# Kernel optimization log

Measured on AMD Instinct MI355X. Metric: run time of the kernel, lower is better.

Reference implementation:

```python
import jax, jax.numpy as jnp
import numpy as np

B = 4096      # graphs
N = 21        # nodes per graph (EEG electrodes)
CIN = 512
H1 = 1024
H2 = 1024
COUT = 512
R = 4         # SE reduction
RANK = 10     # nodevec rank
EPS = 1e-5
THRESH = 0.1


def setup_inputs() -> dict:
    key = jax.random.key(0)
    ks = jax.random.split(key, 16)
    p = lambda i, shape, s=0.02: (jax.random.normal(ks[i], shape, jnp.float32) * s)
    return {
        "x": jax.random.normal(ks[0], (B * N, CIN), jnp.float32),
        "batch": jnp.arange(B * N, dtype=jnp.int32) // N,
        "nodevec1": jax.random.normal(ks[1], (N, RANK), jnp.float32),
        "nodevec2": jax.random.normal(ks[2], (RANK, N), jnp.float32),
        "se_w1": p(3, (CIN, CIN // R), 0.05),
        "se_w2": p(4, (CIN // R, CIN), 0.05),
        "W1": p(5, (CIN, H1)), "b1": jnp.zeros((H1,), jnp.float32),
        "W2": p(6, (H1, H2)), "b2": jnp.zeros((H2,), jnp.float32),
        "W3": p(7, (H2, COUT)), "b3": jnp.zeros((COUT,), jnp.float32),
        "bn1_g": jnp.ones((H1,), jnp.float32), "bn1_b": jnp.zeros((H1,), jnp.float32),
        "bn2_g": jnp.ones((H2,), jnp.float32), "bn2_b": jnp.zeros((H2,), jnp.float32),
        "bn3_g": jnp.ones((COUT,), jnp.float32), "bn3_b": jnp.zeros((COUT,), jnp.float32),
        "rs1_w": p(8, (CIN, H1)), "rs1_b": jnp.zeros((H1,), jnp.float32),
        "fc_w": p(9, (COUT, 2 * COUT)), "fc_b": jnp.zeros((2 * COUT,), jnp.float32),
    }


def _batchnorm(h, g, b):
    # training-mode BN: biased batch stats over the node dimension
    m = h.mean(0)
    v = h.var(0)
    return (h - m) * jax.lax.rsqrt(v + EPS) * g + b


def _gcn(A, h, W, b):
    # GCNConv with precomputed normalized+thresholded weights:
    # out = A_block_diag @ (h @ W) + b, done densely per graph since A is 21x21
    hm = (h @ W).reshape(B, N, -1)                 # [B, N, Cout]
    agg = jnp.einsum('ij,bjc->bic', A, hm)         # message passing per graph
    return agg.reshape(B * N, -1) + b


def _forward(x, batch, nodevec1, nodevec2, se_w1, se_w2,
             W1, b1, W2, b2, W3, b3,
             bn1_g, bn1_b, bn2_g, bn2_b, bn3_g, bn3_b,
             rs1_w, rs1_b, fc_w, fc_b):
    # SE layer on [B, N, C]: channel-wise gating from node-mean features
    x3 = x.reshape(B, N, CIN)
    y = jax.nn.sigmoid(jax.nn.relu(x3.mean(1) @ se_w1) @ se_w2)   # [B, C]
    xg = (x3 * y[:, None, :]).reshape(B * N, CIN)
    # adaptive adjacency: sigmoid(nv1 @ nv2), symmetric normalize, threshold
    adp = jax.nn.sigmoid(nodevec1 @ nodevec2)                      # [N, N]
    at = adp + jnp.eye(N, dtype=adp.dtype)
    deg = at.sum(1)
    dinv = jnp.where(deg > 0, deg ** -0.5, 0.0)
    A = dinv[:, None] * at * dinv[None, :]
    A = jnp.where(A > THRESH, A, 0.0)
    # layer 1 (+ projected residual, BN, relu; dropout omitted = eval)
    h = _batchnorm(_gcn(A, xg, W1, b1), bn1_g, bn1_b) + (xg @ rs1_w + rs1_b)
    h = jax.nn.relu(h)
    # layer 2 (h1 == h2 -> identity residual)
    h = jax.nn.relu(_batchnorm(_gcn(A, h, W2, b2), bn2_g, bn2_b) + h)
    # layer 3
    h = _batchnorm(_gcn(A, h, W3, b3), bn3_g, bn3_b)
    # global mean pool by graph id
    ssum = jax.ops.segment_sum(h, batch, num_segments=B)
    cnt = jax.ops.segment_sum(jnp.ones((h.shape[0], 1), h.dtype), batch, num_segments=B)
    pooled = ssum / cnt
    return pooled @ fc_w + fc_b                                    # [B, 2*COUT]


def reference(x, batch, nodevec1, nodevec2, se_w1, se_w2,
              W1, b1, W2, b2, W3, b3,
              bn1_g, bn1_b, bn2_g, bn2_b, bn3_g, bn3_b,
              rs1_w, rs1_b, fc_w, fc_b):
    return _forward(x, batch, nodevec1, nodevec2, se_w1, se_w2,
                    W1, b1, W2, b2, W3, b3,
                    bn1_g, bn1_b, bn2_g, bn2_b, bn3_g, bn3_b,
                    rs1_w, rs1_b, fc_w, fc_b)
```

## Files before the change

kernel.cpp:

```cpp
#include <hip/hip_runtime.h>

typedef _Float16 f16;
typedef f16 f16x2 __attribute__((ext_vector_type(2)));
typedef f16 f16x8 __attribute__((ext_vector_type(8)));
typedef float f32x4 __attribute__((ext_vector_type(4)));
typedef const void __attribute__((address_space(1)))* gas1;
typedef void __attribute__((address_space(3)))* las3;

#define NB 4096
#define NN 21
#define MROWS (NB*NN)
#define CIN 512
#define H1C 1024
#define H2C 1024
#define COUTC 512

__global__ void k_adj(const float* __restrict__ nv1, const float* __restrict__ nv2,
                      float* __restrict__ Aout) {
  __shared__ float at[21][21];
  __shared__ float dinv[21];
  int t = threadIdx.x;
  if (t < 441) {
    int i = t / 21, j = t % 21;
    float s = 0.f;
    #pragma unroll
    for (int r = 0; r < 10; r++) s += nv1[i*10 + r] * nv2[r*21 + j];
    float v = 1.f / (1.f + expf(-s));
    if (i == j) v += 1.f;
    at[i][j] = v;
  }
  __syncthreads();
  if (t < 21) {
    float d = 0.f;
    #pragma unroll
    for (int j = 0; j < 21; j++) d += at[t][j];
    dinv[t] = d > 0.f ? rsqrtf(d) : 0.f;
  }
  __syncthreads();
  if (t < 441) {
    int i = t / 21, j = t % 21;
    float a = dinv[i] * at[i][j] * dinv[j];
    Aout[t] = a > 0.1f ? a : 0.f;
  }
}

__global__ void k_transpose(const float* __restrict__ src, f16* __restrict__ dst,
                            int K, int N) {
  __shared__ float tile[32][33];
  int n0 = blockIdx.x * 32, k0 = blockIdx.y * 32;
  int tx = threadIdx.x, ty = threadIdx.y;
  #pragma unroll
  for (int i = 0; i < 4; i++)
    tile[ty + 8*i][tx] = src[(size_t)(k0 + ty + 8*i) * N + n0 + tx];
  __syncthreads();
  #pragma unroll
  for (int i = 0; i < 4; i++)
    dst[(size_t)(n0 + ty + 8*i) * K + k0 + tx] = (f16)tile[tx][ty + 8*i];
}

__global__ void k_mean(const float* __restrict__ x, float* __restrict__ xm) {
  int b = blockIdx.x, t = threadIdx.x;
  for (int c = t; c < CIN; c += 256) {
    float s = 0.f;
    #pragma unroll
    for (int n = 0; n < NN; n++) s += x[((size_t)b*NN + n)*CIN + c];
    xm[(size_t)b*CIN + c] = s * (1.f/21.f);
  }
}

__global__ void k_se1(const float* __restrict__ xm, const float* __restrict__ w1,
                      float* __restrict__ y1) {
  __shared__ float row[CIN];
  int b = blockIdx.x, t = threadIdx.x;
  for (int k = t; k < CIN; k += 128) row[k] = xm[(size_t)b*CIN + k];
  __syncthreads();
  float acc = 0.f;
  for (int k = 0; k < CIN; k++) acc += row[k] * w1[(size_t)k*128 + t];
  y1[(size_t)b*128 + t] = fmaxf(acc, 0.f);
}

__global__ void k_se2(const float* __restrict__ y1, const float* __restrict__ w2,
                      float* __restrict__ y) {
  __shared__ float row[128];
  int b = blockIdx.x, t = threadIdx.x;
  if (t < 128) row[t] = y1[(size_t)b*128 + t];
  __syncthreads();
  float acc = 0.f;
  for (int k = 0; k < 128; k++) acc += row[k] * w2[(size_t)k*CIN + t];
  y[(size_t)b*CIN + t] = 1.f / (1.f + expf(-acc));
}

__global__ void k_gate(const float* __restrict__ x, const float* __restrict__ y,
                       f16* __restrict__ xg) {
  size_t i8 = (size_t)blockIdx.x * 256 + threadIdx.x;
  size_t base = i8 * 8;
  int r = (int)(base >> 9);
  int c = (int)(base & 511);
  int b = r / 21;
  const float4* xp = (const float4*)(x + base);
  const float4* yp = (const float4*)(y + (size_t)b*CIN + c);
  float4 a0 = xp[0], a1 = xp[1];
  float4 g0 = yp[0], g1 = yp[1];
  f16x8 o;
  o[0] = (f16)(a0.x * g0.x); o[1] = (f16)(a0.y * g0.y);
  o[2] = (f16)(a0.z * g0.z); o[3] = (f16)(a0.w * g0.w);
  o[4] = (f16)(a1.x * g1.x); o[5] = (f16)(a1.y * g1.y);
  o[6] = (f16)(a1.z * g1.z); o[7] = (f16)(a1.w * g1.w);
  *(f16x8*)(xg + base) = o;
}

#define GBM 128
#define GBN 256
#define BUFB 49152

template<int MODE>
__global__ __launch_bounds__(512, 1)
void k_gemm8(const f16* __restrict__ A, const f16* __restrict__ BT,
             f16* __restrict__ C1, f16* __restrict__ C2,
             const float* __restrict__ bias, float* __restrict__ Cf,
             int N, int K, int lgn) {
  __shared__ __align__(16) char lds[3 * BUFB];
  const int tid = threadIdx.x;
  const int nwg = gridDim.x;
  const int g = blockIdx.x;
  const int swz = (g & 7) * (nwg >> 3) + (g >> 3);
  const int bn = swz & ((1 << lgn) - 1);
  const int bm = swz >> lgn;
  const int lane = tid & 63;
  const int wid = tid >> 6;
  const int wr = wid >> 2;
  const int wc = wid & 3;
  const int fr = lane & 15;
  const int kg = lane >> 4;

  size_t srcOff[6]; int ldsOff[6];
  #pragma unroll
  for (int j = 0; j < 6; j++) {
    int gid = j * 512 + tid;
    if (gid < 1024) {
      int row = gid >> 3, gr = gid & 7;
      int gsw = gr ^ (row & 7);
      srcOff[j] = (size_t)(bm * GBM + row) * K + gsw * 8;
      ldsOff[j] = gid * 16;
    } else {
      int bgid = gid - 1024;
      int row = bgid >> 3, gr = bgid & 7;
      int gsw = gr ^ (row & 7);
      srcOff[j] = (size_t)(bn * GBN + row) * K + gsw * 8;
      ldsOff[j] = 16384 + bgid * 16;
    }
  }

  int aOff[4], axor[4], bOff[4], bxor[4];
  #pragma unroll
  for (int m = 0; m < 4; m++) {
    int row = wr*64 + m*16 + fr;
    aOff[m] = row * 128; axor[m] = row & 7;
  }
  #pragma unroll
  for (int n = 0; n < 4; n++) {
    int row = wc*64 + n*16 + fr;
    bOff[n] = 16384 + row * 128; bxor[n] = row & 7;
  }

  f32x4 acc[4][4];
  #pragma unroll
  for (int m = 0; m < 4; m++)
    #pragma unroll
    for (int n = 0; n < 4; n++)
      #pragma unroll
      for (int r = 0; r < 4; r++) acc[m][n][r] = 0.f;

  auto STAGE3 = [&](int t2, int sbuf, int j0) {
    char* dst = (char*)lds + sbuf * BUFB;
    const size_t kof = (size_t)t2 * 64;
    #pragma unroll
    for (int j = 0; j < 3; j++) {
      int jj = j0 + j;
      const f16* src = (jj < 2 ? A : BT) + srcOff[jj] + kof;
      __builtin_amdgcn_global_load_lds((gas1)src, (las3)(dst + ldsOff[jj]), 16, 0, 0);
    }
  };

  const int NT = K >> 6;
  STAGE3(0, 0, 0); STAGE3(0, 0, 3);
  STAGE3(1, 1, 0); STAGE3(1, 1, 3);
  asm volatile("s_waitcnt vmcnt(6)" ::: "memory");
  asm volatile("s_barrier" ::: "memory");

  for (int t = 0; t < NT; t++) {
    const int cb = t % 3;
    const int sb = (t + 2) % 3;
    const char* rb = (const char*)lds + cb * BUFB;
    const bool ds = (t + 2) < NT;

    f16x8 av[4], bv[4];
    #pragma unroll
    for (int m = 0; m < 4; m++)
      av[m] = *(const f16x8*)(rb + aOff[m] + ((kg ^ axor[m]) << 4));
    #pragma unroll
    for (int n = 0; n < 4; n++)
      bv[n] = *(const f16x8*)(rb + bOff[n] + ((kg ^ bxor[n]) << 4));
    if (ds) STAGE3(t + 2, sb, 0);
    asm volatile("s_barrier" ::: "memory");
    __builtin_amdgcn_s_setprio(1);
    #pragma unroll
    for (int m = 0; m < 4; m++)
      #pragma unroll
      for (int n = 0; n < 4; n++)
        acc[m][n] = __builtin_amdgcn_mfma_f32_16x16x32_f16(av[m], bv[n], acc[m][n], 0, 0, 0);
    __builtin_amdgcn_s_setprio(0);
    asm volatile("s_barrier" ::: "memory");

    #pragma unroll
    for (int m = 0; m < 4; m++)
      av[m] = *(const f16x8*)(rb + aOff[m] + (((4 + kg) ^ axor[m]) << 4));
    #pragma unroll
    for (int n = 0; n < 4; n++)
      bv[n] = *(const f16x8*)(rb + bOff[n] + (((4 + kg) ^ bxor[n]) << 4));
    if (ds) STAGE3(t + 2, sb, 3);
    asm volatile("s_barrier" ::: "memory");
    __builtin_amdgcn_s_setprio(1);
    #pragma unroll
    for (int m = 0; m < 4; m++)
      #pragma unroll
      for (int n = 0; n < 4; n++)
        acc[m][n] = __builtin_amdgcn_mfma_f32_16x16x32_f16(av[m], bv[n], acc[m][n], 0, 0, 0);
    __builtin_amdgcn_s_setprio(0);
    if (ds) asm volatile("s_waitcnt vmcnt(6)" ::: "memory");
    else    asm volatile("s_waitcnt vmcnt(0)" ::: "memory");
    asm volatile("s_barrier" ::: "memory");
  }

  const int crow = bm * GBM + wr * 64 + ((lane >> 4) << 2);
  const int ccol = bn * GBN + wc * 64 + fr;
  if constexpr (MODE == 0) {
    #pragma unroll
    for (int m = 0; m < 4; m++)
      #pragma unroll
      for (int n = 0; n < 4; n++)
        #pragma unroll
        for (int r = 0; r < 4; r++)
          C1[(size_t)(crow + m*16 + r) * N + (ccol + n*16)] = (f16)acc[m][n][r];
  } else if constexpr (MODE == 1) {
    f16* Cp = (bn < 4) ? C1 : C2;
    const int cc = (bn & 3) * 256 + wc * 64 + fr;
    #pragma unroll
    for (int m = 0; m < 4; m++)
      #pragma unroll
      for (int n = 0; n < 4; n++)
        #pragma unroll
        for (int r = 0; r < 4; r++)
          Cp[(size_t)(crow + m*16 + r) * 1024 + (cc + n*16)] = (f16)acc[m][n][r];
  } else {
    #pragma unroll
    for (int n = 0; n < 4; n++) {
      float bb = bias[ccol + n*16];
      #pragma unroll
      for (int m = 0; m < 4; m++)
        #pragma unroll
        for (int r = 0; r < 4; r++)
          Cf[(size_t)(crow + m*16 + r) * N + (ccol + n*16)] = acc[m][n][r] + bb;
    }
  }
}

__global__ __launch_bounds__(256)
void k_mix(f16* __restrict__ t, const float* __restrict__ Aadj,
           float* __restrict__ psum, float* __restrict__ psq, int C) {
  __shared__ float A[441];
  int b = blockIdx.x, tid = threadIdx.x;
  for (int i = tid; i < 441; i += 256) A[i] = Aadj[i];
  __syncthreads();
  int c0 = (blockIdx.y * 256 + tid) * 2;
  size_t base = (size_t)b * NN * C + c0;
  float vx[21], vy[21];
  #pragma unroll
  for (int j = 0; j < 21; j++) {
    f16x2 v = *(const f16x2*)(t + base + (size_t)j * C);
    vx[j] = (float)v[0]; vy[j] = (float)v[1];
  }
  float s0 = 0.f, s1 = 0.f, q0 = 0.f, q1 = 0.f;
  #pragma unroll
  for (int i = 0; i < 21; i++) {
    float a0 = 0.f, a1 = 0.f;
    #pragma unroll
    for (int j = 0; j < 21; j++) {
      float w = A[i*21 + j];
      a0 = fmaf(w, vx[j], a0);
      a1 = fmaf(w, vy[j], a1);
    }
    f16x2 o; o[0] = (f16)a0; o[1] = (f16)a1;
    *(f16x2*)(t + base + (size_t)i * C) = o;
    s0 += a0; s1 += a1;
    q0 = fmaf(a0, a0, q0); q1 = fmaf(a1, a1, q1);
  }
  float2 sv; sv.x = s0; sv.y = s1;
  float2 qv; qv.x = q0; qv.y = q1;
  *(float2*)(psum + (size_t)b * C + c0) = sv;
  *(float2*)(psq  + (size_t)b * C + c0) = qv;
}

__global__ void k_reduce(const float* __restrict__ ps, const float* __restrict__ pq,
                         float* __restrict__ rs, float* __restrict__ rq, int C) {
  int c = blockIdx.x * 256 + threadIdx.x;
  int py = blockIdx.y;
  float s = 0.f, q = 0.f;
  for (int p = py*128; p < py*128 + 128; p++) {
    s += ps[(size_t)p*C + c];
    q += pq[(size_t)p*C + c];
  }
  rs[(size_t)py*C + c] = s;
  rq[(size_t)py*C + c] = q;
}

__global__ void k_bnparams(const float* __restrict__ psum, const float* __restrict__ psq,
                           const float* __restrict__ gamma, const float* __restrict__ beta,
                           const float* __restrict__ resbias,
                           float* __restrict__ scale, float* __restrict__ shift,
                           int C, int npart) {
  int c = blockIdx.x * 256 + threadIdx.x;
  float s = 0.f, q = 0.f;
  for (int p = 0; p < npart; p++) { s += psum[(size_t)p*C + c]; q += psq[(size_t)p*C + c]; }
  const float Minv = 1.f / (float)MROWS;
  float mean = s * Minv;
  float var = q * Minv - mean * mean;
  float sc = gamma[c] * rsqrtf(var + 1e-5f);
  float sh = beta[c] - mean * sc;
  if (resbias) sh += resbias[c];
  scale[c] = sc; shift[c] = sh;
}

__global__ void k_finalize(const f16* __restrict__ g, const f16* __restrict__ res,
                           f16* __restrict__ dst, const float* __restrict__ scale,
                           const float* __restrict__ shift, int cmask) {
  size_t i8 = (size_t)blockIdx.x * 256 + threadIdx.x;
  size_t base = i8 * 8;
  int c = (int)(base & (size_t)cmask);
  f16x8 gv = *(const f16x8*)(g + base);
  f16x8 rv = *(const f16x8*)(res + base);
  f16x8 o;
  #pragma unroll
  for (int j = 0; j < 8; j++) {
    float v = (float)gv[j] * scale[c + j] + shift[c + j] + (float)rv[j];
    o[j] = (f16)fmaxf(v, 0.f);
  }
  *(f16x8*)(dst + base) = o;
}

__global__ void k_pool(const f16* __restrict__ g3, const float* __restrict__ scale,
                       const float* __restrict__ shift, f16* __restrict__ pooled) {
  int b = blockIdx.x, t = threadIdx.x;
  for (int c = t; c < COUTC; c += 256) {
    float s = 0.f;
    #pragma unroll
    for (int n = 0; n < NN; n++) s += (float)g3[((size_t)b*NN + n)*COUTC + c];
    pooled[(size_t)b*COUTC + c] = (f16)((s * (1.f/21.f)) * scale[c] + shift[c]);
  }
}

extern "C" void kernel_launch(void* const* d_in, const int* in_sizes, int n_in,
                              void* d_out, int out_size, void* d_ws, size_t ws_size,
                              hipStream_t stream) {
  const float* x     = (const float*)d_in[0];
  const float* nv1   = (const float*)d_in[2];
  const float* nv2   = (const float*)d_in[3];
  const float* se_w1 = (const float*)d_in[4];
  const float* se_w2 = (const float*)d_in[5];
  const float* W1    = (const float*)d_in[6];
  const float* W2    = (const float*)d_in[8];
  const float* W3    = (const float*)d_in[10];
  const float* bn1g  = (const float*)d_in[12];
  const float* bn1b  = (const float*)d_in[13];
  const float* bn2g  = (const float*)d_in[14];
  const float* bn2b  = (const float*)d_in[15];
  const float* bn3g  = (const float*)d_in[16];
  const float* bn3b  = (const float*)d_in[17];
  const float* rs1w  = (const float*)d_in[18];
  const float* rs1b  = (const float*)d_in[19];
  const float* fcw   = (const float*)d_in[20];
  const float* fcb   = (const float*)d_in[21];
  float* out = (float*)d_out;

  char* ws = (char*)d_ws;
  size_t off = 0;
  auto alloc = [&](size_t bytes) -> char* {
    char* p = ws + off;
    off = (off + bytes + 255) & ~(size_t)255;
    return p;
  };

  float* A_adj = (float*)alloc(441 * 4);
  f16* W1R  = (f16*)alloc((size_t)2048 * CIN * 2);
  f16* W2T  = (f16*)alloc((size_t)H2C * H1C * 2);
  f16* W3T  = (f16*)alloc((size_t)COUTC * H2C * 2);
  f16* FCWT = (f16*)alloc((size_t)1024 * COUTC * 2);
  float* xm = (float*)alloc((size_t)NB * CIN * 4);
  float* y1 = (float*)alloc((size_t)NB * 128 * 4);
  float* yv = (float*)alloc((size_t)NB * CIN * 4);
  float* psum = (float*)alloc((size_t)NB * 1024 * 4);
  float* psq  = (float*)alloc((size_t)NB * 1024 * 4);
  float* rsum = (float*)alloc((size_t)32 * 1024 * 4);
  float* rsq  = (float*)alloc((size_t)32 * 1024 * 4);
  float* sc1 = (float*)alloc(1024 * 4);
  float* sh1 = (float*)alloc(1024 * 4);
  float* sc2 = (float*)alloc(1024 * 4);
  float* sh2 = (float*)alloc(1024 * 4);
  float* sc3 = (float*)alloc(1024 * 4);
  float* sh3 = (float*)alloc(1024 * 4);
  f16* pooled = (f16*)alloc((size_t)NB * COUTC * 2);
  f16* P1 = (f16*)alloc((size_t)MROWS * 512 * 2);
  f16* P2 = (f16*)alloc((size_t)MROWS * 1024 * 2);
  f16* P3 = (f16*)alloc((size_t)MROWS * 1024 * 2);
  (void)ws_size; (void)in_sizes; (void)n_in; (void)out_size;

  k_adj<<<1, 512, 0, stream>>>(nv1, nv2, A_adj);
  k_transpose<<<dim3(32, 16), dim3(32, 8), 0, stream>>>(W1,   W1R,                    512, 1024);
  k_transpose<<<dim3(32, 16), dim3(32, 8), 0, stream>>>(rs1w, W1R + (size_t)1024*512, 512, 1024);
  k_transpose<<<dim3(32, 32), dim3(32, 8), 0, stream>>>(W2,   W2T,  1024, 1024);
  k_transpose<<<dim3(16, 32), dim3(32, 8), 0, stream>>>(W3,   W3T,  1024, 512);
  k_transpose<<<dim3(32, 16), dim3(32, 8), 0, stream>>>(fcw,  FCWT, 512, 1024);

  k_mean<<<NB, 256, 0, stream>>>(x, xm);
  k_se1<<<NB, 128, 0, stream>>>(xm, se_w1, y1);
  k_se2<<<NB, 512, 0, stream>>>(y1, se_w2, yv);
  k_gate<<<21504, 256, 0, stream>>>(x, yv, P1);

  k_gemm8<1><<<672*8, 512, 0, stream>>>(P1, W1R, P2, P3, nullptr, nullptr, 2048, 512, 3);
  k_mix<<<dim3(NB, 2), 256, 0, stream>>>(P2, A_adj, psum, psq, 1024);
  k_reduce<<<dim3(4, 32), 256, 0, stream>>>(psum, psq, rsum, rsq, 1024);
  k_bnparams<<<4, 256, 0, stream>>>(rsum, rsq, bn1g, bn1b, rs1b, sc1, sh1, 1024, 32);
  k_finalize<<<43008, 256, 0, stream>>>(P2, P3, P3, sc1, sh1, 1023);

  k_gemm8<0><<<672*4, 512, 0, stream>>>(P3, W2T, P2, nullptr, nullptr, nullptr, 1024, 1024, 2);
  k_mix<<<dim3(NB, 2), 256, 0, stream>>>(P2, A_adj, psum, psq, 1024);
  k_reduce<<<dim3(4, 32), 256, 0, stream>>>(psum, psq, rsum, rsq, 1024);
  k_bnparams<<<4, 256, 0, stream>>>(rsum, rsq, bn2g, bn2b, nullptr, sc2, sh2, 1024, 32);
  k_finalize<<<43008, 256, 0, stream>>>(P2, P3, P2, sc2, sh2, 1023);

  k_gemm8<0><<<672*2, 512, 0, stream>>>(P2, W3T, P1, nullptr, nullptr, nullptr, 512, 1024, 1);
  k_mix<<<dim3(NB, 1), 256, 0, stream>>>(P1, A_adj, psum, psq, 512);
  k_reduce<<<dim3(2, 32), 256, 0, stream>>>(psum, psq, rsum, rsq, 512);
  k_bnparams<<<2, 256, 0, stream>>>(rsum, rsq, bn3g, bn3b, nullptr, sc3, sh3, 512, 32);

  k_pool<<<NB, 256, 0, stream>>>(P1, sc3, sh3, pooled);
  k_gemm8<2><<<32*4, 512, 0, stream>>>(pooled, FCWT, nullptr, nullptr, fcb, out, 1024, 512, 2);
}
```

Measured before the change: 1.215 ms.

## Reassociate adjacency mix before GEMMs, fuse BN stats into GEMM epilogue, pipeline LDS reads

Uses A(hW) = (Ah)W to apply the 21x21 adjacency mix before the GEMM on the narrower input: in place on the 512-wide gated input for layer 1, and fused with BN-finalize/relu in a new k_finmix for layer 3. The GEMM epilogue now computes per-tile column sums and sums of squares for the batch-norm statistics, so the separate mix+stats passes for layers 1 and 3 go away. The gemm main loop is restructured to double-buffer LDS fragment reads across half-steps with fewer barriers. Layer 1 now runs as two separate GEMMs instead of one concatenated GEMM. Fp16 rounding happens at different points, which may shift numerics slightly.

```diff
diff --git a/kernel.cpp b/kernel.cpp
--- a/kernel.cpp
+++ b/kernel.cpp
@@ -11,9 +11,6 @@
 #define NN 21
 #define MROWS (NB*NN)
 #define CIN 512
-#define H1C 1024
-#define H2C 1024
-#define COUTC 512
 
 __global__ void k_adj(const float* __restrict__ nv1, const float* __restrict__ nv2,
                       float* __restrict__ Aout) {
@@ -116,9 +113,9 @@
 template<int MODE>
 __global__ __launch_bounds__(512, 1)
 void k_gemm8(const f16* __restrict__ A, const f16* __restrict__ BT,
-             f16* __restrict__ C1, f16* __restrict__ C2,
-             const float* __restrict__ bias, float* __restrict__ Cf,
-             int N, int K, int lgn) {
+             f16* __restrict__ C1, const float* __restrict__ bias,
+             float* __restrict__ Cf, float* __restrict__ psum,
+             float* __restrict__ psq, int N, int K, int lgn) {
   __shared__ __align__(16) char lds[3 * BUFB];
   const int tid = threadIdx.x;
   const int nwg = gridDim.x;
@@ -181,60 +178,70 @@
       __builtin_amdgcn_global_load_lds((gas1)src, (las3)(dst + ldsOff[jj]), 16, 0, 0);
     }
   };
-
+  auto READF = [&](f16x8* avv, f16x8* bvv, const char* rb, int s) {
+    #pragma unroll
+    for (int m = 0; m < 4; m++)
+      avv[m] = *(const f16x8*)(rb + aOff[m] + (((s*4 + kg) ^ axor[m]) << 4));
+    #pragma unroll
+    for (int n = 0; n < 4; n++)
+      bvv[n] = *(const f16x8*)(rb + bOff[n] + (((s*4 + kg) ^ bxor[n]) << 4));
+  };
+
+  f16x8 av0[4], bv0[4], av1[4], bv1[4];
   const int NT = K >> 6;
   STAGE3(0, 0, 0); STAGE3(0, 0, 3);
   STAGE3(1, 1, 0); STAGE3(1, 1, 3);
   asm volatile("s_waitcnt vmcnt(6)" ::: "memory");
   asm volatile("s_barrier" ::: "memory");
+  READF(av0, bv0, (const char*)lds, 0);
 
   for (int t = 0; t < NT; t++) {
-    const int cb = t % 3;
+    const char* rb  = (const char*)lds + (t % 3) * BUFB;
+    const char* rbn = (const char*)lds + ((t + 1) % 3) * BUFB;
     const int sb = (t + 2) % 3;
-    const char* rb = (const char*)lds + cb * BUFB;
-    const bool ds = (t + 2) < NT;
-
-    f16x8 av[4], bv[4];
+    const bool stg  = (t + 2) < NT;
+    const bool more = (t + 1) < NT;
+
+    if (stg) STAGE3(t + 2, sb, 0);
+    READF(av1, bv1, rb, 1);
+    __builtin_amdgcn_s_setprio(1);
     #pragma unroll
     for (int m = 0; m < 4; m++)
-      av[m] = *(const f16x8*)(rb + aOff[m] + ((kg ^ axor[m]) << 4));
-    #pragma unroll
-    for (int n = 0; n < 4; n++)
-      bv[n] = *(const f16x8*)(rb + bOff[n] + ((kg ^ bxor[n]) << 4));
-    if (ds) STAGE3(t + 2, sb, 0);
-    asm volatile("s_barrier" ::: "memory");
+      #pragma unroll
+      for (int n = 0; n < 4; n++)
+        acc[m][n] = __builtin_amdgcn_mfma_f32_16x16x32_f16(av0[m], bv0[n], acc[m][n], 0, 0, 0);
+    __builtin_amdgcn_s_setprio(0);
+    if (stg) STAGE3(t + 2, sb, 3);
+
+    if (more) {
+      if (stg) asm volatile("s_waitcnt vmcnt(6)" ::: "memory");
+      else     asm volatile("s_waitcnt vmcnt(0)" ::: "memory");
+      asm volatile("s_barrier" ::: "memory");
+      READF(av0, bv0, rbn, 0);
+    }
     __builtin_amdgcn_s_setprio(1);
     #pragma unroll
     for (int m = 0; m < 4; m++)
       #pragma unroll
       for (int n = 0; n < 4; n++)
-        acc[m][n] = __builtin_amdgcn_mfma_f32_16x16x32_f16(av[m], bv[n], acc[m][n], 0, 0, 0);
+        acc[m][n] = __builtin_amdgcn_mfma_f32_16x16x32_f16(av1[m], bv1[n], acc[m][n], 0, 0, 0);
     __builtin_amdgcn_s_setprio(0);
     asm volatile("s_barrier" ::: "memory");
-
-    #pragma unroll
-    for (int m = 0; m < 4; m++)
-      av[m] = *(const f16x8*)(rb + aOff[m] + (((4 + kg) ^ axor[m]) << 4));
-    #pragma unroll
-    for (int n = 0; n < 4; n++)
-      bv[n] = *(const f16x8*)(rb + bOff[n] + (((4 + kg) ^ bxor[n]) << 4));
-    if (ds) STAGE3(t + 2, sb, 3);
-    asm volatile("s_barrier" ::: "memory");
-    __builtin_amdgcn_s_setprio(1);
-    #pragma unroll
-    for (int m = 0; m < 4; m++)
-      #pragma unroll
-      for (int n = 0; n < 4; n++)
-        acc[m][n] = __builtin_amdgcn_mfma_f32_16x16x32_f16(av[m], bv[n], acc[m][n], 0, 0, 0);
-    __builtin_amdgcn_s_setprio(0);
-    if (ds) asm volatile("s_waitcnt vmcnt(6)" ::: "memory");
-    else    asm volatile("s_waitcnt vmcnt(0)" ::: "memory");
-    asm volatile("s_barrier" ::: "memory");
   }
 
   const int crow = bm * GBM + wr * 64 + ((lane >> 4) << 2);
   const int ccol = bn * GBN + wc * 64 + fr;
-  if constexpr (MODE == 0) {
+  if constexpr (MODE == 2) {
+    #pragma unroll
+    for (int n = 0; n < 4; n++) {
+      float bb = bias[ccol + n*16];
+      #pragma unroll
+      for (int m = 0; m < 4; m++)
+        #pragma unroll
+        for (int r = 0; r < 4; r++)
+          Cf[(size_t)(crow + m*16 + r) * N + (ccol + n*16)] = acc[m][n][r] + bb;
+    }
+  } else {
     #pragma unroll
     for (int m = 0; m < 4; m++)
       #pragma unroll
@@ -242,26 +249,60 @@
         #pragma unroll
         for (int r = 0; r < 4; r++)
           C1[(size_t)(crow + m*16 + r) * N + (ccol + n*16)] = (f16)acc[m][n][r];
-  } else if constexpr (MODE == 1) {
-    f16* Cp = (bn < 4) ? C1 : C2;
-    const int cc = (bn & 3) * 256 + wc * 64 + fr;
-    #pragma unroll
-    for (int m = 0; m < 4; m++)
-      #pragma unroll
-      for (int n = 0; n < 4; n++)
-        #pragma unroll
-        for (int r = 0; r < 4; r++)
-          Cp[(size_t)(crow + m*16 + r) * 1024 + (cc + n*16)] = (f16)acc[m][n][r];
-  } else {
+  }
+  if constexpr (MODE == 1) {
+    float s[4], q[4];
     #pragma unroll
     for (int n = 0; n < 4; n++) {
-      float bb = bias[ccol + n*16];
+      float ss = 0.f, qq = 0.f;
       #pragma unroll
       for (int m = 0; m < 4; m++)
         #pragma unroll
-        for (int r = 0; r < 4; r++)
-          Cf[(size_t)(crow + m*16 + r) * N + (ccol + n*16)] = acc[m][n][r] + bb;
-    }
+        for (int r = 0; r < 4; r++) { float v = acc[m][n][r]; ss += v; qq = fmaf(v, v, qq); }
+      s[n] = ss; q[n] = qq;
+    }
+    #pragma unroll
+    for (int n = 0; n < 4; n++) {
+      s[n] += __shfl_xor(s[n], 16); s[n] += __shfl_xor(s[n], 32);
+      q[n] += __shfl_xor(q[n], 16); q[n] += __shfl_xor(q[n], 32);
+    }
+    float* wred = (float*)lds;
+    if ((lane >> 4) == 0) {
+      #pragma unroll
+      for (int n = 0; n < 4; n++) {
+        wred[wr*256 + wc*64 + n*16 + fr]       = s[n];
+        wred[512 + wr*256 + wc*64 + n*16 + fr] = q[n];
+      }
+    }
+    __syncthreads();
+    if (tid < 256) {
+      psum[(size_t)bm * N + bn*256 + tid] = wred[tid]       + wred[256 + tid];
+      psq [(size_t)bm * N + bn*256 + tid] = wred[512 + tid] + wred[768 + tid];
+    }
+  }
+}
+
+__global__ __launch_bounds__(256)
+void k_mixip(f16* __restrict__ t, const float* __restrict__ Aadj) {
+  __shared__ float A[441];
+  int b = blockIdx.x, tid = threadIdx.x;
+  for (int i = tid; i < 441; i += 256) A[i] = Aadj[i];
+  __syncthreads();
+  int c0 = tid * 2;
+  size_t base = (size_t)b * NN * 512 + c0;
+  float vx[21], vy[21];
+  #pragma unroll
+  for (int j = 0; j < 21; j++) {
+    f16x2 v = *(const f16x2*)(t + base + (size_t)j * 512);
+    vx[j] = (float)v[0]; vy[j] = (float)v[1];
+  }
+  #pragma unroll
+  for (int i = 0; i < 21; i++) {
+    float a0 = 0.f, a1 = 0.f;
+    #pragma unroll
+    for (int j = 0; j < 21; j++) { float w = A[i*21+j]; a0 = fmaf(w, vx[j], a0); a1 = fmaf(w, vy[j], a1); }
+    f16x2 o; o[0] = (f16)a0; o[1] = (f16)a1;
+    *(f16x2*)(t + base + (size_t)i * 512) = o;
   }
 }
 
@@ -302,11 +343,12 @@
 }
 
 __global__ void k_reduce(const float* __restrict__ ps, const float* __restrict__ pq,
-                         float* __restrict__ rs, float* __restrict__ rq, int C) {
+                         float* __restrict__ rs, float* __restrict__ rq,
+                         int C, int per) {
   int c = blockIdx.x * 256 + threadIdx.x;
   int py = blockIdx.y;
   float s = 0.f, q = 0.f;
-  for (int p = py*128; p < py*128 + 128; p++) {
+  for (int p = py*per; p < py*per + per; p++) {
     s += ps[(size_t)p*C + c];
     q += pq[(size_t)p*C + c];
   }
@@ -331,8 +373,8 @@
   scale[c] = sc; shift[c] = sh;
 }
 
-__global__ void k_finalize(const f16* __restrict__ g, const f16* __restrict__ res,
-                           f16* __restrict__ dst, const float* __restrict__ scale,
+__global__ void k_finalize(const f16* __restrict__ g, const f16* res,
+                           f16* dst, const float* __restrict__ scale,
                            const float* __restrict__ shift, int cmask) {
   size_t i8 = (size_t)blockIdx.x * 256 + threadIdx.x;
   size_t base = i8 * 8;
@@ -348,14 +390,48 @@
   *(f16x8*)(dst + base) = o;
 }
 
+__global__ __launch_bounds__(256)
+void k_finmix(const f16* t, const f16* res, f16* hout, f16* hmix,
+              const float* __restrict__ scale, const float* __restrict__ shift,
+              const float* __restrict__ Aadj, int C) {
+  __shared__ float A[441];
+  int b = blockIdx.x, tid = threadIdx.x;
+  for (int i = tid; i < 441; i += 256) A[i] = Aadj[i];
+  __syncthreads();
+  int c0 = (blockIdx.y * 256 + tid) * 2;
+  float scx = scale[c0], scy = scale[c0+1];
+  float shx = shift[c0], shy = shift[c0+1];
+  size_t base = (size_t)b * NN * C + c0;
+  float hx[21], hy[21];
+  #pragma unroll
+  for (int j = 0; j < 21; j++) {
+    f16x2 tv = *(const f16x2*)(t + base + (size_t)j*C);
+    f16x2 rv = *(const f16x2*)(res + base + (size_t)j*C);
+    hx[j] = fmaxf((float)tv[0]*scx + shx + (float)rv[0], 0.f);
+    hy[j] = fmaxf((float)tv[1]*scy + shy + (float)rv[1], 0.f);
+    if (hout) {
+      f16x2 o; o[0] = (f16)hx[j]; o[1] = (f16)hy[j];
+      *(f16x2*)(hout + base + (size_t)j*C) = o;
+    }
+  }
+  #pragma unroll
+  for (int i = 0; i < 21; i++) {
+    float a0 = 0.f, a1 = 0.f;
+    #pragma unroll
+    for (int j = 0; j < 21; j++) { float w = A[i*21+j]; a0 = fmaf(w, hx[j], a0); a1 = fmaf(w, hy[j], a1); }
+    f16x2 o; o[0] = (f16)a0; o[1] = (f16)a1;
+    *(f16x2*)(hmix + base + (size_t)i*C) = o;
+  }
+}
+
 __global__ void k_pool(const f16* __restrict__ g3, const float* __restrict__ scale,
                        const float* __restrict__ shift, f16* __restrict__ pooled) {
   int b = blockIdx.x, t = threadIdx.x;
-  for (int c = t; c < COUTC; c += 256) {
+  for (int c = t; c < 512; c += 256) {
     float s = 0.f;
     #pragma unroll
-    for (int n = 0; n < NN; n++) s += (float)g3[((size_t)b*NN + n)*COUTC + c];
-    pooled[(size_t)b*COUTC + c] = (f16)((s * (1.f/21.f)) * scale[c] + shift[c]);
+    for (int n = 0; n < NN; n++) s += (float)g3[((size_t)b*NN + n)*512 + c];
+    pooled[(size_t)b*512 + c] = (f16)((s * (1.f/21.f)) * scale[c] + shift[c]);
   }
 }
 
@@ -391,15 +467,14 @@
   };
 
   float* A_adj = (float*)alloc(441 * 4);
-  f16* W1R  = (f16*)alloc((size_t)2048 * CIN * 2);
-  f16* W2T  = (f16*)alloc((size_t)H2C * H1C * 2);
-  f16* W3T  = (f16*)alloc((size_t)COUTC * H2C * 2);
-  f16* FCWT = (f16*)alloc((size_t)1024 * COUTC * 2);
-  float* xm = (float*)alloc((size_t)NB * CIN * 4);
-  float* y1 = (float*)alloc((size_t)NB * 128 * 4);
-  float* yv = (float*)alloc((size_t)NB * CIN * 4);
+  f16* W1T  = (f16*)alloc((size_t)1024 * 512 * 2);
+  f16* RS1T = (f16*)alloc((size_t)1024 * 512 * 2);
+  f16* W2T  = (f16*)alloc((size_t)1024 * 1024 * 2);
+  f16* W3T  = (f16*)alloc((size_t)512 * 1024 * 2);
+  f16* FCWT = (f16*)alloc((size_t)1024 * 512 * 2);
   float* psum = (float*)alloc((size_t)NB * 1024 * 4);
   float* psq  = (float*)alloc((size_t)NB * 1024 * 4);
+  float* y1   = (float*)alloc((size_t)NB * 128 * 4);
   float* rsum = (float*)alloc((size_t)32 * 1024 * 4);
   float* rsq  = (float*)alloc((size_t)32 * 1024 * 4);
   float* sc1 = (float*)alloc(1024 * 4);
@@ -408,15 +483,17 @@
   float* sh2 = (float*)alloc(1024 * 4);
   float* sc3 = (float*)alloc(1024 * 4);
   float* sh3 = (float*)alloc(1024 * 4);
-  f16* pooled = (f16*)alloc((size_t)NB * COUTC * 2);
-  f16* P1 = (f16*)alloc((size_t)MROWS * 512 * 2);
-  f16* P2 = (f16*)alloc((size_t)MROWS * 1024 * 2);
-  f16* P3 = (f16*)alloc((size_t)MROWS * 1024 * 2);
+  f16* pooled = (f16*)alloc((size_t)NB * 512 * 2);
+  f16* G = (f16*)alloc((size_t)MROWS * 512 * 2);
+  f16* R = (f16*)alloc((size_t)MROWS * 1024 * 2);
+  f16* T = (f16*)alloc((size_t)MROWS * 1024 * 2);
+  float* xm = psum;
+  float* yv = psq;
   (void)ws_size; (void)in_sizes; (void)n_in; (void)out_size;
 
   k_adj<<<1, 512, 0, stream>>>(nv1, nv2, A_adj);
-  k_transpose<<<dim3(32, 16), dim3(32, 8), 0, stream>>>(W1,   W1R,                    512, 1024);
-  k_transpose<<<dim3(32, 16), dim3(32, 8), 0, stream>>>(rs1w, W1R + (size_t)1024*512, 512, 1024);
+  k_transpose<<<dim3(32, 16), dim3(32, 8), 0, stream>>>(W1,   W1T,  512, 1024);
+  k_transpose<<<dim3(32, 16), dim3(32, 8), 0, stream>>>(rs1w, RS1T, 512, 1024);
   k_transpose<<<dim3(32, 32), dim3(32, 8), 0, stream>>>(W2,   W2T,  1024, 1024);
   k_transpose<<<dim3(16, 32), dim3(32, 8), 0, stream>>>(W3,   W3T,  1024, 512);
   k_transpose<<<dim3(32, 16), dim3(32, 8), 0, stream>>>(fcw,  FCWT, 512, 1024);
@@ -424,25 +501,25 @@
   k_mean<<<NB, 256, 0, stream>>>(x, xm);
   k_se1<<<NB, 128, 0, stream>>>(xm, se_w1, y1);
   k_se2<<<NB, 512, 0, stream>>>(y1, se_w2, yv);
-  k_gate<<<21504, 256, 0, stream>>>(x, yv, P1);
-
-  k_gemm8<1><<<672*8, 512, 0, stream>>>(P1, W1R, P2, P3, nullptr, nullptr, 2048, 512, 3);
-  k_mix<<<dim3(NB, 2), 256, 0, stream>>>(P2, A_adj, psum, psq, 1024);
-  k_reduce<<<dim3(4, 32), 256, 0, stream>>>(psum, psq, rsum, rsq, 1024);
+  k_gate<<<21504, 256, 0, stream>>>(x, yv, G);
+
+  k_gemm8<0><<<672*4, 512, 0, stream>>>(G, RS1T, R, nullptr, nullptr, nullptr, nullptr, 1024, 512, 2);
+  k_mixip<<<NB, 256, 0, stream>>>(G, A_adj);
+  k_gemm8<1><<<672*4, 512, 0, stream>>>(G, W1T, T, nullptr, nullptr, psum, psq, 1024, 512, 2);
+  k_reduce<<<dim3(4, 32), 256, 0, stream>>>(psum, psq, rsum, rsq, 1024, 21);
   k_bnparams<<<4, 256, 0, stream>>>(rsum, rsq, bn1g, bn1b, rs1b, sc1, sh1, 1024, 32);
-  k_finalize<<<43008, 256, 0, stream>>>(P2, P3, P3, sc1, sh1, 1023);
-
-  k_gemm8<0><<<672*4, 512, 0, stream>>>(P3, W2T, P2, nullptr, nullptr, nullptr, 1024, 1024, 2);
-  k_mix<<<dim3(NB, 2), 256, 0, stream>>>(P2, A_adj, psum, psq, 1024);
-  k_reduce<<<dim3(4, 32), 256, 0, stream>>>(psum, psq, rsum, rsq, 1024);
+  k_finalize<<<43008, 256, 0, stream>>>(T, R, R, sc1, sh1, 1023);
+
+  k_gemm8<0><<<672*4, 512, 0, stream>>>(R, W2T, T, nullptr, nullptr, nullptr, nullptr, 1024, 1024, 2);
+  k_mix<<<dim3(NB, 2), 256, 0, stream>>>(T, A_adj, psum, psq, 1024);
+  k_reduce<<<dim3(4, 32), 256, 0, stream>>>(psum, psq, rsum, rsq, 1024, 128);
   k_bnparams<<<4, 256, 0, stream>>>(rsum, rsq, bn2g, bn2b, nullptr, sc2, sh2, 1024, 32);
-  k_finalize<<<43008, 256, 0, stream>>>(P2, P3, P2, sc2, sh2, 1023);
-
-  k_gemm8<0><<<672*2, 512, 0, stream>>>(P2, W3T, P1, nullptr, nullptr, nullptr, 512, 1024, 1);
-  k_mix<<<dim3(NB, 1), 256, 0, stream>>>(P1, A_adj, psum, psq, 512);
-  k_reduce<<<dim3(2, 32), 256, 0, stream>>>(psum, psq, rsum, rsq, 512);
+  k_finmix<<<dim3(NB, 2), 256, 0, stream>>>(T, R, nullptr, T, sc2, sh2, A_adj, 1024);
+
+  k_gemm8<1><<<672*2, 512, 0, stream>>>(T, W3T, G, nullptr, nullptr, psum, psq, 512, 1024, 1);
+  k_reduce<<<dim3(2, 32), 256, 0, stream>>>(psum, psq, rsum, rsq, 512, 21);
   k_bnparams<<<2, 256, 0, stream>>>(rsum, rsq, bn3g, bn3b, nullptr, sc3, sh3, 512, 32);
 
-  k_pool<<<NB, 256, 0, stream>>>(P1, sc3, sh3, pooled);
-  k_gemm8<2><<<32*4, 512, 0, stream>>>(pooled, FCWT, nullptr, nullptr, fcb, out, 1024, 512, 2);
-}
+  k_pool<<<NB, 256, 0, stream>>>(G, sc3, sh3, pooled);
+  k_gemm8<2><<<32*4, 512, 0, stream>>>(pooled, FCWT, nullptr, fcb, out, nullptr, nullptr, 1024, 512, 2);
+}
```

Result: faster. 1.186 ms (-2.4%).
